# Kernel optimization log

Hardware: AMD Instinct MI355X
Metric: run time of the kernel (lower is better)

Reference implementation:

```python
import jax, jax.numpy as jnp
import numpy as np

N = 50000      # nodes
E = 800000     # edges (before self-loops)
IN = 64        # in_channels
HID = 128      # hidden
HEADS = 4
C = HID // HEADS  # per-head dim = 32
EPS_BN = 1e-5


def setup_inputs() -> dict:
    key = jax.random.key(0)
    ks = jax.random.split(key, 40)
    f32 = jnp.float32
    def rn(i, shape, s=0.05):
        return jax.random.normal(ks[i], shape, f32) * s
    def un(i, shape, lo=0.5, hi=1.5):
        return jax.random.uniform(ks[i], shape, f32, lo, hi)
    inp = {
        'x': jax.random.normal(ks[0], (N, IN), f32),
        'edge_index': jax.random.randint(ks[1], (2, E), 0, N, jnp.int64),
        # pre: Linear(IN, HID) + BatchNorm1d(HID)
        'W_pre': rn(2, (IN, HID)), 'b_pre': rn(3, (HID,)),
        'g_pre': un(4, (HID,)), 'be_pre': rn(5, (HID,)),
        'm_pre': rn(6, (HID,), 0.1), 'v_pre': un(7, (HID,)),
        # gat1 (GATv2Conv): lin_l, lin_r, att, bias
        'Wl1': rn(8, (HID, HID)), 'bl1': rn(9, (HID,)),
        'Wr1': rn(10, (HID, HID)), 'br1': rn(11, (HID,)),
        'att1': rn(12, (HEADS, C)), 'bias1': rn(13, (HID,)),
        'g1': un(14, (HID,)), 'be1': rn(15, (HID,)),
        'm1': rn(16, (HID,), 0.1), 'v1': un(17, (HID,)),
        # gat2
        'Wl2': rn(18, (HID, HID)), 'bl2': rn(19, (HID,)),
        'Wr2': rn(20, (HID, HID)), 'br2': rn(21, (HID,)),
        'att2': rn(22, (HEADS, C)), 'bias2': rn(23, (HID,)),
        'g2': un(24, (HID,)), 'be2': rn(25, (HID,)),
        'm2': rn(26, (HID,), 0.1), 'v2': un(27, (HID,)),
        # out head: Linear(HID, HID//2) -> LeakyReLU -> Linear(HID//2, 1)
        'Wo1': rn(28, (HID, HID // 2)), 'bo1': rn(29, (HID // 2,)),
        'Wo2': rn(30, (HID // 2, 1)), 'bo2': rn(31, (1,)),
    }
    return inp


def _bn(x, g, b, m, v):
    # eval-mode BatchNorm1d with running stats
    return (x - m) * jax.lax.rsqrt(v + EPS_BN) * g + b


def _gatv2(x, src, dst, Wl, bl, Wr, br, att, bias):
    # PyG GATv2Conv, concat=True, negative_slope=0.2, eval (no dropout)
    n = x.shape[0]
    xl = (x @ Wl + bl).reshape(n, HEADS, C)   # messages from source
    xr = (x @ Wr + br).reshape(n, HEADS, C)   # target side
    xj = xl[src]                              # [E2, H, C] gather
    s = jax.nn.leaky_relu(xr[dst] + xj, 0.2)
    logits = jnp.einsum('ehc,hc->eh', s, att)  # [E2, H]
    # segment softmax over destination nodes
    mx = jax.ops.segment_max(logits, dst, num_segments=n)
    e = jnp.exp(logits - mx[dst])
    den = jax.ops.segment_sum(e, dst, num_segments=n)
    alpha = e / (den[dst] + 1e-16)
    out = jax.ops.segment_sum(xj * alpha[:, :, None], dst, num_segments=n)
    return out.reshape(n, HID) + bias


def reference(x, edge_index,
              W_pre, b_pre, g_pre, be_pre, m_pre, v_pre,
              Wl1, bl1, Wr1, br1, att1, bias1, g1, be1, m1, v1,
              Wl2, bl2, Wr2, br2, att2, bias2, g2, be2, m2, v2,
              Wo1, bo1, Wo2, bo2):
    n = x.shape[0]
    # add self loops (PyG GATv2Conv default add_self_loops=True)
    loop = jnp.arange(n, dtype=edge_index.dtype)
    src = jnp.concatenate([edge_index[0], loop])
    dst = jnp.concatenate([edge_index[1], loop])

    x = jax.nn.leaky_relu(_bn(x @ W_pre + b_pre, g_pre, be_pre, m_pre, v_pre), 0.1)
    h = x
    x = _gatv2(x, src, dst, Wl1, bl1, Wr1, br1, att1, bias1)
    x = jax.nn.leaky_relu(_bn(x, g1, be1, m1, v1), 0.1) + h
    h = x
    x = _gatv2(x, src, dst, Wl2, bl2, Wr2, br2, att2, bias2)
    x = jax.nn.leaky_relu(_bn(x, g2, be2, m2, v2), 0.1) + h
    x = jax.nn.leaky_relu(x @ Wo1 + bo1, 0.1)
    return x @ Wo2 + bo2
```

## Files before the change

kernel.cpp:

```cpp
#include <hip/hip_runtime.h>
#include <hip/hip_bf16.h>
#include <hip/hip_fp16.h>

#define NN 50000
#define EE 800000
#define SCAN_B 196

typedef unsigned int uint;
typedef unsigned short ushort;
typedef __attribute__((ext_vector_type(8))) short s16x8;
typedef __attribute__((ext_vector_type(4))) float f32x4;
typedef __attribute__((ext_vector_type(2))) _Float16 h16x2;

__device__ __forceinline__ float lrelu(float x, float s){ return fmaxf(x, x * s); }

__device__ __forceinline__ ushort bf16_rne(float x){
  uint u = __float_as_uint(x);
  return (ushort)((u + 0x7FFFu + ((u >> 16) & 1u)) >> 16);
}
__device__ __forceinline__ float bf16f(ushort h){ return __uint_as_float(((uint)h) << 16); }

__device__ __forceinline__ float dpp_add4(float x){
  int v = __float_as_int(x), t;
  t = __builtin_amdgcn_update_dpp(0, v, 0xB1, 0xF, 0xF, true);
  v = __float_as_int(__int_as_float(v) + __int_as_float(t));
  t = __builtin_amdgcn_update_dpp(0, v, 0x4E, 0xF, 0xF, true);
  v = __float_as_int(__int_as_float(v) + __int_as_float(t));
  return __int_as_float(v);
}


__global__ void detect_kernel(const int* __restrict__ ei, int* __restrict__ flag){
  __shared__ int any;
  if (threadIdx.x == 0) any = 0;
  __syncthreads();
  if (ei[2 * threadIdx.x + 1] != 0) atomicOr(&any, 1);
  __syncthreads();
  if (threadIdx.x == 0) *flag = (any == 0) ? 1 : 0;
}

__global__ void zero1_kernel(int* __restrict__ a, int n){
  int i = blockIdx.x * blockDim.x + threadIdx.x;
  if (i < n) a[i] = 0;
}

__global__ void count_kernel(const int* __restrict__ ei, const int* __restrict__ flag,
                             int* __restrict__ deg){
  int e = blockIdx.x * blockDim.x + threadIdx.x;
  if (e >= EE) return;
  int d;
  if (*flag){
    const long long* eil = (const long long*)ei;
    d = (int)eil[EE + e];
  } else {
    d = ei[EE + e];
  }
  atomicAdd(&deg[d], 1);
}

__global__ void scan1_kernel(const int* __restrict__ deg, int* __restrict__ rowptr,
                             int* __restrict__ bsum){
  __shared__ int tmp[256];
  int tid = threadIdx.x;
  int idx = blockIdx.x * 256 + tid;
  int v = (idx < NN) ? deg[idx] : 0;
  tmp[tid] = v;
  __syncthreads();
  for (int off = 1; off < 256; off <<= 1){
    int t = (tid >= off) ? tmp[tid - off] : 0;
    __syncthreads();
    tmp[tid] += t;
    __syncthreads();
  }
  if (idx < NN) rowptr[idx] = tmp[tid] - v;
  if (tid == 255) bsum[blockIdx.x] = tmp[255];
}

__global__ void scan2_kernel(const int* __restrict__ bsum, int* __restrict__ boff,
                             int* __restrict__ rowptr){
  __shared__ int tmp[256];
  int tid = threadIdx.x;
  int v = (tid < SCAN_B) ? bsum[tid] : 0;
  tmp[tid] = v;
  __syncthreads();
  for (int off = 1; off < 256; off <<= 1){
    int t = (tid >= off) ? tmp[tid - off] : 0;
    __syncthreads();
    tmp[tid] += t;
    __syncthreads();
  }
  if (tid < SCAN_B) boff[tid] = tmp[tid] - v;
  if (tid == 255) rowptr[NN] = tmp[255];
}

__global__ void scan3_kernel(int* __restrict__ rowptr, const int* __restrict__ boff,
                             int* __restrict__ deg){
  int i = blockIdx.x * 256 + threadIdx.x;
  if (i < NN){ rowptr[i] += boff[blockIdx.x]; deg[i] = 0; }
}

__global__ void scatter_kernel(const int* __restrict__ ei, const int* __restrict__ flag,
                               const int* __restrict__ rowptr, int* __restrict__ cursor,
                               int* __restrict__ csr_src){
  int e = blockIdx.x * blockDim.x + threadIdx.x;
  if (e >= EE) return;
  int s, d;
  if (*flag){
    const long long* eil = (const long long*)ei;
    s = (int)eil[e];
    d = (int)eil[EE + e];
  } else {
    s = ei[e];
    d = ei[EE + e];
  }
  int pos = atomicAdd(&cursor[d], 1);
  csr_src[rowptr[d] + pos] = s;
}

__global__ void prep_w_kernel(const float* __restrict__ w0, const float* __restrict__ w1,
                              const float* __restrict__ w2, const float* __restrict__ w3,
                              const float* __restrict__ w4, const float* __restrict__ w5,
                              ushort* __restrict__ wt){
  int gid = blockIdx.x * 256 + threadIdx.x;
  if (gid >= 81920) return;
  const int KK[6]    = {64, 128, 128, 128, 128, 128};
  const int CC[6]    = {128, 128, 128, 128, 128, 64};
  const int cumel[7] = {0, 8192, 24576, 40960, 57344, 73728, 81920};
  int j = 0;
  while (gid >= cumel[j + 1]) j++;
  int local = gid - cumel[j];
  int K = KK[j], C = CC[j];
  int k = local / C, c = local % C;
  const float* src = (j == 0) ? w0 : (j == 1) ? w1 : (j == 2) ? w2 : (j == 3) ? w3 : (j == 4) ? w4 : w5;
  wt[cumel[j] + c * K + k] = bf16_rne(src[local]);
}

template<int KIN, int NOUT, int EPI, bool DUAL>
__launch_bounds__(256, 2)
__global__ void mfma_gemm_kernel(const float* __restrict__ A,
                                 const ushort* __restrict__ Wt, const float* __restrict__ bias,
                                 const ushort* __restrict__ Wt2, const float* __restrict__ bias2,
                                 const float* __restrict__ bn_g, const float* __restrict__ bn_b,
                                 const float* __restrict__ bn_m, const float* __restrict__ bn_v,
                                 ushort* __restrict__ OUTH, float* __restrict__ OUTF, int n){
  constexpr int KF = KIN / 32;
  constexpr int NF = NOUT / 16;
  constexpr int WELEM = KIN * NOUT;
  constexpr int NW = DUAL ? 2 : 1;
  __shared__ ushort sW[NW * WELEM];
  const int tid  = threadIdx.x;
  const int wave = tid >> 6, lane = tid & 63;
  const int fr = lane & 15;
  const int kg = lane >> 4;
  const int r0 = blockIdx.x * 128 + wave * 32;

  for (int i = tid; i < NW * WELEM / 8; i += 256){
    const ushort* src = (i * 8 < WELEM) ? (Wt + i * 8) : (Wt2 + (i * 8 - WELEM));
    uint4 w = *reinterpret_cast<const uint4*>(src);
    uint b = (uint)i * 16u;
    uint sb = b ^ (((b >> 8) & 7u) << 4);
    *reinterpret_cast<uint4*>((char*)sW + sb) = w;
  }

  const int ar0 = min(r0 + fr,      n - 1);
  const int ar1 = min(r0 + 16 + fr, n - 1);

  s16x8 ah[2][KF], al[2][KF];
  #pragma unroll
  for (int kf = 0; kf < KF; kf++){
    const float* p0 = A + (size_t)ar0 * KIN + kf * 32 + kg * 8;
    const float* p1 = A + (size_t)ar1 * KIN + kf * 32 + kg * 8;
    float4 a0 = *reinterpret_cast<const float4*>(p0);
    float4 b0 = *reinterpret_cast<const float4*>(p0 + 4);
    float4 a1 = *reinterpret_cast<const float4*>(p1);
    float4 b1 = *reinterpret_cast<const float4*>(p1 + 4);
    float f0[8] = {a0.x, a0.y, a0.z, a0.w, b0.x, b0.y, b0.z, b0.w};
    float f1[8] = {a1.x, a1.y, a1.z, a1.w, b1.x, b1.y, b1.z, b1.w};
    #pragma unroll
    for (int j = 0; j < 8; j++){
      ushort h0 = bf16_rne(f0[j]);
      ah[0][kf][j] = (short)h0;
      al[0][kf][j] = (short)bf16_rne(f0[j] - bf16f(h0));
      ushort h1 = bf16_rne(f1[j]);
      ah[1][kf][j] = (short)h1;
      al[1][kf][j] = (short)bf16_rne(f1[j] - bf16f(h1));
    }
  }
  __syncthreads();

  f32x4 acc[2][NF];

#define GEMM_PHASE(PH)                                                                    \
  {                                                                                       \
    _Pragma("unroll")                                                                     \
    for (int nf = 0; nf < NF; nf++){                                                      \
      s16x8 wh[KF];                                                                       \
      _Pragma("unroll")                                                                   \
      for (int kf = 0; kf < KF; kf++){                                                    \
        uint b = (uint)(((PH) * WELEM + (nf * 16 + fr) * KIN + kf * 32 + kg * 8) * 2);    \
        wh[kf] = *reinterpret_cast<const s16x8*>((const char*)sW + (b ^ (((b >> 8) & 7u) << 4))); \
      }                                                                                   \
      _Pragma("unroll")                                                                   \
      for (int kf = 0; kf < KF; kf++){                                                    \
        acc[0][nf] = __builtin_amdgcn_mfma_f32_16x16x32_bf16(ah[0][kf], wh[kf], acc[0][nf], 0, 0, 0); \
        acc[1][nf] = __builtin_amdgcn_mfma_f32_16x16x32_bf16(ah[1][kf], wh[kf], acc[1][nf], 0, 0, 0); \
        acc[0][nf] = __builtin_amdgcn_mfma_f32_16x16x32_bf16(al[0][kf], wh[kf], acc[0][nf], 0, 0, 0); \
        acc[1][nf] = __builtin_amdgcn_mfma_f32_16x16x32_bf16(al[1][kf], wh[kf], acc[1][nf], 0, 0, 0); \
      }                                                                                   \
    }                                                                                     \
  }

  #pragma unroll
  for (int nf = 0; nf < NF; nf++){ acc[0][nf] = (f32x4){0.f,0.f,0.f,0.f}; acc[1][nf] = (f32x4){0.f,0.f,0.f,0.f}; }
  GEMM_PHASE(0)

  #pragma unroll
  for (int nf = 0; nf < NF; nf++){
    int c = nf * 16 + fr;
    float bb = bias[c];
    float g_ = 0.f, b_ = 0.f, m_ = 0.f, v_ = 0.f;
    if (EPI == 1){ g_ = bn_g[c]; b_ = bn_b[c]; m_ = bn_m[c]; v_ = bn_v[c]; }
    #pragma unroll
    for (int rg = 0; rg < 2; rg++){
      #pragma unroll
      for (int i = 0; i < 4; i++){
        int gr = r0 + rg * 16 + kg * 4 + i;
        if (gr < n){
          float v = acc[rg][nf][i] + bb;
          if (EPI == 1){
            v = (v - m_) * rsqrtf(v_ + 1e-5f) * g_ + b_;
            v = lrelu(v, 0.1f);
          }
          if (EPI == 2){ v = lrelu(v, 0.1f); }
          if (DUAL){
            __half hv = __float2half(v);
            OUTH[(size_t)gr * NOUT + c] = *reinterpret_cast<ushort*>(&hv);
          } else {
            OUTF[(size_t)gr * NOUT + c] = v;
          }
        }
      }
    }
  }

  if (DUAL){
    #pragma unroll
    for (int nf = 0; nf < NF; nf++){ acc[0][nf] = (f32x4){0.f,0.f,0.f,0.f}; acc[1][nf] = (f32x4){0.f,0.f,0.f,0.f}; }
    GEMM_PHASE(1)
    #pragma unroll
    for (int nf = 0; nf < NF; nf++){
      int c = nf * 16 + fr;
      float bb = bias2[c];
      #pragma unroll
      for (int rg = 0; rg < 2; rg++){
        #pragma unroll
        for (int i = 0; i < 4; i++){
          int gr = r0 + rg * 16 + kg * 4 + i;
          if (gr < n) OUTF[(size_t)gr * NOUT + c] = acc[rg][nf][i] + bb;
        }
      }
    }
  }
#undef GEMM_PHASE
}

__global__ void gat_edge_kernel(const uint* __restrict__ XLh, const float* __restrict__ XR,
                                const float* __restrict__ att, const float* __restrict__ bias,
                                const float* __restrict__ bn_g, const float* __restrict__ bn_b,
                                const float* __restrict__ bn_m, const float* __restrict__ bn_v,
                                const float* __restrict__ H, float* __restrict__ OUT,
                                const int* __restrict__ rowptr, const int* __restrict__ csr_src,
                                int n){
  const int wid  = (int)((blockIdx.x * blockDim.x + threadIdx.x) >> 6);
  const int lane = threadIdx.x & 63;
  const int nb = wid * 4;
  if (nb >= n) return;
  const int g  = lane >> 4;
  const int c4 = lane & 15;
  const int cb = c4 * 8;
  const int d  = min(nb + g, n - 1);
  const float L2E = 1.44269504f;

  float4 xr0 = *reinterpret_cast<const float4*>(XR + (size_t)d * 128 + cb);
  float4 xr1 = *reinterpret_cast<const float4*>(XR + (size_t)d * 128 + cb + 4);
  float4 at0 = *reinterpret_cast<const float4*>(att + cb);
  float4 at1 = *reinterpret_cast<const float4*>(att + cb + 4);
  __half2 xrh[4] = { __floats2half2_rn(xr0.x, xr0.y), __floats2half2_rn(xr0.z, xr0.w),
                     __floats2half2_rn(xr1.x, xr1.y), __floats2half2_rn(xr1.z, xr1.w) };
  __half2 ath[4] = { __floats2half2_rn(at0.x * L2E, at0.y * L2E), __floats2half2_rn(at0.z * L2E, at0.w * L2E),
                     __floats2half2_rn(at1.x * L2E, at1.y * L2E), __floats2half2_rn(at1.z * L2E, at1.w * L2E) };
  const __half2 c06 = __float2half2_rn(0.6f);
  const __half2 c04 = __float2half2_rn(0.4f);

  float den = 0.f;
  float O[8] = {0.f,0.f,0.f,0.f,0.f,0.f,0.f,0.f};

  const int start = rowptr[d];
  const int cnt = rowptr[d + 1] - start + 1;
  const int* __restrict__ base = csr_src + start - 1;

  int mx = cnt;
  mx = max(mx, __shfl_xor(mx, 16));
  mx = max(mx, __shfl_xor(mx, 32));

  auto IDX = [&](int s) -> int {
    int c = min(s, cnt - 1);
    return (c == 0) ? d : base[c];
  };
  auto ROW = [&](int si) -> uint4 {
    return *reinterpret_cast<const uint4*>(XLh + (size_t)si * 64 + c4 * 4);
  };

  auto PROC = [&](uint4 cur, int s){
    const bool valid = s < cnt;
    __half2 x0 = *reinterpret_cast<__half2*>(&cur.x);
    __half2 x1 = *reinterpret_cast<__half2*>(&cur.y);
    __half2 x2 = *reinterpret_cast<__half2*>(&cur.z);
    __half2 x3 = *reinterpret_cast<__half2*>(&cur.w);
    __half2 s0 = __hadd2(xrh[0], x0);
    __half2 s1 = __hadd2(xrh[1], x1);
    __half2 s2 = __hadd2(xrh[2], x2);
    __half2 s3 = __hadd2(xrh[3], x3);
    uint a0u = *reinterpret_cast<uint*>(&s0) & 0x7FFF7FFFu;
    uint a1u = *reinterpret_cast<uint*>(&s1) & 0x7FFF7FFFu;
    uint a2u = *reinterpret_cast<uint*>(&s2) & 0x7FFF7FFFu;
    uint a3u = *reinterpret_cast<uint*>(&s3) & 0x7FFF7FFFu;
    __half2 l0 = __hfma2(c06, s0, __hmul2(c04, *reinterpret_cast<__half2*>(&a0u)));
    __half2 l1 = __hfma2(c06, s1, __hmul2(c04, *reinterpret_cast<__half2*>(&a1u)));
    __half2 l2 = __hfma2(c06, s2, __hmul2(c04, *reinterpret_cast<__half2*>(&a2u)));
    __half2 l3 = __hfma2(c06, s3, __hmul2(c04, *reinterpret_cast<__half2*>(&a3u)));
#if __has_builtin(__builtin_amdgcn_fdot2)
    float acc = __builtin_amdgcn_fdot2(*reinterpret_cast<h16x2*>(&ath[0]), *reinterpret_cast<h16x2*>(&l0), 0.f, false);
    acc = __builtin_amdgcn_fdot2(*reinterpret_cast<h16x2*>(&ath[1]), *reinterpret_cast<h16x2*>(&l1), acc, false);
    acc = __builtin_amdgcn_fdot2(*reinterpret_cast<h16x2*>(&ath[2]), *reinterpret_cast<h16x2*>(&l2), acc, false);
    acc = __builtin_amdgcn_fdot2(*reinterpret_cast<h16x2*>(&ath[3]), *reinterpret_cast<h16x2*>(&l3), acc, false);
#else
    float2 q0 = __half22float2(l0), q1 = __half22float2(l1), q2 = __half22float2(l2), q3 = __half22float2(l3);
    float2 p0 = __half22float2(ath[0]), p1 = __half22float2(ath[1]), p2 = __half22float2(ath[2]), p3 = __half22float2(ath[3]);
    float acc = q0.x*p0.x + q0.y*p0.y + q1.x*p1.x + q1.y*p1.y
              + q2.x*p2.x + q2.y*p2.y + q3.x*p3.x + q3.y*p3.y;
#endif
    acc = dpp_add4(acc);
    float w = valid ? exp2f(acc) : 0.f;
    den += w;
    float2 f0 = __half22float2(x0), f1 = __half22float2(x1);
    float2 f2 = __half22float2(x2), f3 = __half22float2(x3);
    O[0] = fmaf(w, f0.x, O[0]);  O[1] = fmaf(w, f0.y, O[1]);
    O[2] = fmaf(w, f1.x, O[2]);  O[3] = fmaf(w, f1.y, O[3]);
    O[4] = fmaf(w, f2.x, O[4]);  O[5] = fmaf(w, f2.y, O[5]);
    O[6] = fmaf(w, f3.x, O[6]);  O[7] = fmaf(w, f3.y, O[7]);
  };

  uint4 r0 = ROW(IDX(0)), r1 = ROW(IDX(1)), r2 = ROW(IDX(2));
  for (int s = 0; s < mx; s++){
    int j3 = IDX(s + 3);
    PROC(r0, s);
    r0 = r1; r1 = r2; r2 = ROW(j3);
  }

  {
    float inv = 1.f / (den + 1e-16f);
    float4 bi0 = *reinterpret_cast<const float4*>(bias + cb);
    float4 bi1 = *reinterpret_cast<const float4*>(bias + cb + 4);
    float4 g0 = *reinterpret_cast<const float4*>(bn_g + cb);
    float4 g1 = *reinterpret_cast<const float4*>(bn_g + cb + 4);
    float4 bb0 = *reinterpret_cast<const float4*>(bn_b + cb);
    float4 bb1 = *reinterpret_cast<const float4*>(bn_b + cb + 4);
    float4 mm0 = *reinterpret_cast<const float4*>(bn_m + cb);
    float4 mm1 = *reinterpret_cast<const float4*>(bn_m + cb + 4);
    float4 vv0 = *reinterpret_cast<const float4*>(bn_v + cb);
    float4 vv1 = *reinterpret_cast<const float4*>(bn_v + cb + 4);
    float4 h0 = *reinterpret_cast<const float4*>(H + (size_t)d * 128 + cb);
    float4 h1 = *reinterpret_cast<const float4*>(H + (size_t)d * 128 + cb + 4);
    float bi[8] = {bi0.x,bi0.y,bi0.z,bi0.w,bi1.x,bi1.y,bi1.z,bi1.w};
    float gg[8] = {g0.x,g0.y,g0.z,g0.w,g1.x,g1.y,g1.z,g1.w};
    float bbv[8]= {bb0.x,bb0.y,bb0.z,bb0.w,bb1.x,bb1.y,bb1.z,bb1.w};
    float mmv[8]= {mm0.x,mm0.y,mm0.z,mm0.w,mm1.x,mm1.y,mm1.z,mm1.w};
    float vvv[8]= {vv0.x,vv0.y,vv0.z,vv0.w,vv1.x,vv1.y,vv1.z,vv1.w};
    float hh[8] = {h0.x,h0.y,h0.z,h0.w,h1.x,h1.y,h1.z,h1.w};
    float r[8];
    #pragma unroll
    for (int j = 0; j < 8; j++){
      float v = O[j] * inv + bi[j];
      v = (v - mmv[j]) * rsqrtf(vvv[j] + 1e-5f) * gg[j] + bbv[j];
      r[j] = lrelu(v, 0.1f) + hh[j];
    }
    *reinterpret_cast<float4*>(OUT + (size_t)d * 128 + cb)     = make_float4(r[0], r[1], r[2], r[3]);
    *reinterpret_cast<float4*>(OUT + (size_t)d * 128 + cb + 4) = make_float4(r[4], r[5], r[6], r[7]);
  }
}

__global__ void out2_kernel(const float* __restrict__ Hin, const float* __restrict__ Wo2,
                            const float* __restrict__ bo2, float* __restrict__ out, int n){
  int wid  = (int)((blockIdx.x * blockDim.x + threadIdx.x) >> 6);
  int lane = threadIdx.x & 63;
  if (wid >= n) return;
  float p = Hin[(long)wid * 64 + lane] * Wo2[lane];
  #pragma unroll
  for (int off = 1; off < 64; off <<= 1) p += __shfl_xor(p, off);
  if (lane == 0) out[wid] = p + bo2[0];
}

extern "C" void kernel_launch(void* const* d_in, const int* in_sizes, int n_in,
                              void* d_out, int out_size, void* d_ws, size_t ws_size,
                              hipStream_t stream) {
  const float* x     = (const float*)d_in[0];
  const int*   ei    = (const int*)  d_in[1];
  const float* W_pre = (const float*)d_in[2];
  const float* b_pre = (const float*)d_in[3];
  const float* g_pre = (const float*)d_in[4];
  const float* be_pre= (const float*)d_in[5];
  const float* m_pre = (const float*)d_in[6];
  const float* v_pre = (const float*)d_in[7];
  const float* Wl1  = (const float*)d_in[8];
  const float* bl1  = (const float*)d_in[9];
  const float* Wr1  = (const float*)d_in[10];
  const float* br1  = (const float*)d_in[11];
  const float* att1 = (const float*)d_in[12];
  const float* bias1= (const float*)d_in[13];
  const float* g1   = (const float*)d_in[14];
  const float* be1  = (const float*)d_in[15];
  const float* m1   = (const float*)d_in[16];
  const float* v1   = (const float*)d_in[17];
  const float* Wl2  = (const float*)d_in[18];
  const float* bl2  = (const float*)d_in[19];
  const float* Wr2  = (const float*)d_in[20];
  const float* br2  = (const float*)d_in[21];
  const float* att2 = (const float*)d_in[22];
  const float* bias2= (const float*)d_in[23];
  const float* g2   = (const float*)d_in[24];
  const float* be2  = (const float*)d_in[25];
  const float* m2   = (const float*)d_in[26];
  const float* v2   = (const float*)d_in[27];
  const float* Wo1  = (const float*)d_in[28];
  const float* bo1  = (const float*)d_in[29];
  const float* Wo2  = (const float*)d_in[30];
  const float* bo2  = (const float*)d_in[31];
  float* out = (float*)d_out;
  char*  ws  = (char*)d_ws;

  float*  buf0 = (float*)(ws + 0);
  float*  buf2 = (float*)(ws + 25600000);
  uint*   hbuf = (uint*) (ws + 51200000);
  int* rowptr = (int*)(ws + 64000000);
  int* deg    = (int*)(ws + 64200448);
  int* bsum   = (int*)(ws + 64400448);
  int* boff   = (int*)(ws + 64401472);
  int* csr    = (int*)(ws + 64600448);
  int* flag   = (int*)(ws + 67800448);
  ushort* wt  = (ushort*)(ws + 68000000);

  const ushort* wtPre = wt;
  const ushort* wtL1  = wt + 8192;
  const ushort* wtR1  = wt + 24576;
  const ushort* wtL2  = wt + 40960;
  const ushort* wtR2  = wt + 57344;
  const ushort* wtO1  = wt + 73728;

  detect_kernel<<<1, 256, 0, stream>>>(ei, flag);
  zero1_kernel<<<SCAN_B, 256, 0, stream>>>(deg, NN);
  count_kernel<<<(EE + 255) / 256, 256, 0, stream>>>(ei, flag, deg);
  scan1_kernel<<<SCAN_B, 256, 0, stream>>>(deg, rowptr, bsum);
  scan2_kernel<<<1, 256, 0, stream>>>(bsum, boff, rowptr);
  scan3_kernel<<<SCAN_B, 256, 0, stream>>>(rowptr, boff, deg);
  scatter_kernel<<<(EE + 255) / 256, 256, 0, stream>>>(ei, flag, rowptr, deg, csr);

  prep_w_kernel<<<320, 256, 0, stream>>>(W_pre, Wl1, Wr1, Wl2, Wr2, Wo1, wt);

  const int GB = (NN + 127) / 128;
  const int GW = (NN + 15) / 16;

  mfma_gemm_kernel<64, 128, 1, false><<<GB, 256, 0, stream>>>(
      x, wtPre, b_pre, nullptr, nullptr,
      g_pre, be_pre, m_pre, v_pre, nullptr, buf0, NN);
  mfma_gemm_kernel<128, 128, 0, true><<<GB, 256, 0, stream>>>(
      buf0, wtL1, bl1, wtR1, br1,
      nullptr, nullptr, nullptr, nullptr, (ushort*)hbuf, buf2, NN);
  gat_edge_kernel<<<GW, 256, 0, stream>>>(hbuf, buf2, att1, bias1, g1, be1, m1, v1,
                                          buf0 , buf2 , rowptr, csr, NN);
  mfma_gemm_kernel<128, 128, 0, true><<<GB, 256, 0, stream>>>(
      buf2, wtL2, bl2, wtR2, br2,
      nullptr, nullptr, nullptr, nullptr, (ushort*)hbuf, buf0, NN);
  gat_edge_kernel<<<GW, 256, 0, stream>>>(hbuf, buf0, att2, bias2, g2, be2, m2, v2,
                                          buf2 , buf0 , rowptr, csr, NN);
  mfma_gemm_kernel<128, 64, 2, false><<<GB, 256, 0, stream>>>(
      buf0, wtO1, bo1, nullptr, nullptr,
      nullptr, nullptr, nullptr, nullptr, nullptr, buf2, NN);
  out2_kernel<<<(NN + 3) / 4, 256, 0, stream>>>(buf2, Wo2, bo2, out, NN);
}
```

Baseline: 283.6 us.

## Build CSR via two-level bucketed scatter instead of global atomic scatter

Replaces the single global-atomic CSR scatter with a two-pass scheme. Edges are first binned into buckets of 32 destination nodes through a bucket histogram, a scan and a binning pass that writes (src,dst) pairs. Then one block per bucket scatters its edges into the CSR using shared-memory atomics. This aims to cut contended global atomics and scattered writes, at the cost of extra kernel launches, an extra 6.4MB pair buffer round trip, and a serial single-block bucket scan.

```diff
diff --git a/kernel.cpp b/kernel.cpp
--- a/kernel.cpp
+++ b/kernel.cpp
@@ -5,6 +5,7 @@
 #define NN 50000
 #define EE 800000
 #define SCAN_B 196
+#define NB 1563
 
 typedef unsigned int uint;
 typedef unsigned short ushort;
@@ -39,13 +40,14 @@
   if (threadIdx.x == 0) *flag = (any == 0) ? 1 : 0;
 }
 
-__global__ void zero1_kernel(int* __restrict__ a, int n){
+__global__ void zero2_kernel(int* __restrict__ a, int na, int* __restrict__ b, int nbv){
   int i = blockIdx.x * blockDim.x + threadIdx.x;
-  if (i < n) a[i] = 0;
+  if (i < na) a[i] = 0;
+  if (i < nbv) b[i] = 0;
 }
 
 __global__ void count_kernel(const int* __restrict__ ei, const int* __restrict__ flag,
-                             int* __restrict__ deg){
+                             int* __restrict__ deg, int* __restrict__ bhist){
   int e = blockIdx.x * blockDim.x + threadIdx.x;
   if (e >= EE) return;
   int d;
@@ -56,6 +58,7 @@
     d = ei[EE + e];
   }
   atomicAdd(&deg[d], 1);
+  atomicAdd(&bhist[d >> 5], 1);
 }
 
 __global__ void scan1_kernel(const int* __restrict__ deg, int* __restrict__ rowptr,
@@ -93,15 +96,39 @@
   if (tid == 255) rowptr[NN] = tmp[255];
 }
 
-__global__ void scan3_kernel(int* __restrict__ rowptr, const int* __restrict__ boff,
-                             int* __restrict__ deg){
+__global__ void scan3_kernel(int* __restrict__ rowptr, const int* __restrict__ boff){
   int i = blockIdx.x * 256 + threadIdx.x;
-  if (i < NN){ rowptr[i] += boff[blockIdx.x]; deg[i] = 0; }
-}
-
-__global__ void scatter_kernel(const int* __restrict__ ei, const int* __restrict__ flag,
-                               const int* __restrict__ rowptr, int* __restrict__ cursor,
-                               int* __restrict__ csr_src){
+  if (i < NN) rowptr[i] += boff[blockIdx.x];
+}
+
+__global__ void bscan_kernel(const int* __restrict__ bhist, int* __restrict__ bboff,
+                             int* __restrict__ bcur){
+  __shared__ int tmp[256];
+  __shared__ int carry_s;
+  int tid = threadIdx.x;
+  if (tid == 0) carry_s = 0;
+  __syncthreads();
+  for (int base = 0; base < NB; base += 256){
+    int idx = base + tid;
+    int v = (idx < NB) ? bhist[idx] : 0;
+    tmp[tid] = v;
+    __syncthreads();
+    for (int off = 1; off < 256; off <<= 1){
+      int t = (tid >= off) ? tmp[tid - off] : 0;
+      __syncthreads();
+      tmp[tid] += t;
+      __syncthreads();
+    }
+    if (idx < NB){ int ex = carry_s + tmp[tid] - v; bboff[idx] = ex; bcur[idx] = ex; }
+    __syncthreads();
+    if (tid == 0) carry_s += tmp[255];
+    __syncthreads();
+  }
+  if (tid == 0) bboff[NB] = carry_s;
+}
+
+__global__ void bin_kernel(const int* __restrict__ ei, const int* __restrict__ flag,
+                           int* __restrict__ bcur, uint2* __restrict__ bpair){
   int e = blockIdx.x * blockDim.x + threadIdx.x;
   if (e >= EE) return;
   int s, d;
@@ -113,8 +140,26 @@
     s = ei[e];
     d = ei[EE + e];
   }
-  int pos = atomicAdd(&cursor[d], 1);
-  csr_src[rowptr[d] + pos] = s;
+  int pos = atomicAdd(&bcur[d >> 5], 1);
+  bpair[pos] = make_uint2((uint)s, (uint)d);
+}
+
+__global__ void bucket_scatter_kernel(const uint2* __restrict__ bpair,
+                                      const int* __restrict__ bboff,
+                                      const int* __restrict__ rowptr,
+                                      int* __restrict__ csr){
+  __shared__ int lcur[32];
+  if (threadIdx.x < 32) lcur[threadIdx.x] = 0;
+  __syncthreads();
+  const int b = blockIdx.x;
+  const int base = b << 5;
+  const int s0 = bboff[b], s1 = bboff[b + 1];
+  for (int i = s0 + (int)threadIdx.x; i < s1; i += 256){
+    uint2 p = bpair[i];
+    int d = (int)p.y;
+    int pos = atomicAdd(&lcur[d - base], 1);
+    csr[rowptr[d] + pos] = (int)p.x;
+  }
 }
 
 __global__ void prep_w_kernel(const float* __restrict__ w0, const float* __restrict__ w1,
@@ -449,6 +494,10 @@
   int* csr    = (int*)(ws + 64600448);
   int* flag   = (int*)(ws + 67800448);
   ushort* wt  = (ushort*)(ws + 68000000);
+  int* bhist  = (int*)(ws + 68200000);
+  int* bboff  = (int*)(ws + 68210000);
+  int* bcur   = (int*)(ws + 68220000);
+  uint2* bpair= (uint2*)(ws + 68230016);
 
   const ushort* wtPre = wt;
   const ushort* wtL1  = wt + 8192;
@@ -458,12 +507,14 @@
   const ushort* wtO1  = wt + 73728;
 
   detect_kernel<<<1, 256, 0, stream>>>(ei, flag);
-  zero1_kernel<<<SCAN_B, 256, 0, stream>>>(deg, NN);
-  count_kernel<<<(EE + 255) / 256, 256, 0, stream>>>(ei, flag, deg);
+  zero2_kernel<<<SCAN_B, 256, 0, stream>>>(deg, NN, bhist, NB);
+  count_kernel<<<(EE + 255) / 256, 256, 0, stream>>>(ei, flag, deg, bhist);
   scan1_kernel<<<SCAN_B, 256, 0, stream>>>(deg, rowptr, bsum);
   scan2_kernel<<<1, 256, 0, stream>>>(bsum, boff, rowptr);
-  scan3_kernel<<<SCAN_B, 256, 0, stream>>>(rowptr, boff, deg);
-  scatter_kernel<<<(EE + 255) / 256, 256, 0, stream>>>(ei, flag, rowptr, deg, csr);
+  scan3_kernel<<<SCAN_B, 256, 0, stream>>>(rowptr, boff);
+  bscan_kernel<<<1, 256, 0, stream>>>(bhist, bboff, bcur);
+  bin_kernel<<<(EE + 255) / 256, 256, 0, stream>>>(ei, flag, bcur, bpair);
+  bucket_scatter_kernel<<<NB, 256, 0, stream>>>(bpair, bboff, rowptr, csr);
 
   prep_w_kernel<<<320, 256, 0, stream>>>(W_pre, Wl1, Wr1, Wl2, Wr2, Wo1, wt);
 
```

Result: slower. 492.8 us (+73.8%).
